# Kernel tuning notes

Hardware: AMD Instinct MI355X
Metric: run time of the kernel (lower is better)

## Reference

```python
import jax, jax.numpy as jnp
import numpy as np

B, T, D, K = 32, 2048, 1024, 31


def setup_inputs() -> dict:
    key = jax.random.key(0)
    ks = jax.random.split(key, 8)
    query = jax.random.normal(ks[0], (B, D), dtype=jnp.float32)
    memory = jax.random.normal(ks[1], (B, T, D), dtype=jnp.float32)
    prev_attn = jax.nn.softmax(jax.random.normal(ks[2], (B, T)), axis=-1).astype(jnp.float32)
    cum_attn = jax.random.uniform(ks[3], (B, T), dtype=jnp.float32)
    mask = jax.random.bernoulli(ks[4], 0.2, (B, T))
    mask = mask.at[:, 0].set(False)  # keep at least one valid position per row
    scale = 0.02
    Wq = jax.random.normal(ks[5], (D, D), dtype=jnp.float32) * scale    # torch Linear weight [out,in]
    Wm = jax.random.normal(ks[6], (D, D), dtype=jnp.float32) * scale
    k2 = jax.random.split(ks[7], 2)
    Wloc = jax.random.normal(k2[0], (D, 2, K), dtype=jnp.float32) * scale  # Conv1d weight [out_ch,in_ch,k]
    v = jax.random.normal(k2[1], (D,), dtype=jnp.float32) * scale          # Linear(d_model,1) weight squeezed
    return {"query": query, "memory": memory, "prev_attn": prev_attn,
            "cum_attn": cum_attn, "mask": mask,
            "Wq": Wq, "Wm": Wm, "Wloc": Wloc, "v": v}


def reference(query, memory, prev_attn, cum_attn, mask, Wq, Wm, Wloc, v):
    pad = Wloc.shape[-1] // 2
    # location features: [B,2,T] conv -> [B,D,T] -> [B,T,D]
    loc_in = jnp.stack([prev_attn, cum_attn], axis=1)
    loc = jax.lax.conv_general_dilated(
        loc_in, Wloc, window_strides=(1,), padding=[(pad, pad)],
        dimension_numbers=("NCW", "OIW", "NCW"))
    loc = jnp.transpose(loc, (0, 2, 1))                 # [B,T,D]
    q = (query @ Wq.T)[:, None, :]                      # [B,1,D]
    m = jnp.einsum("btd,ed->bte", memory, Wm)           # [B,T,D]
    e = jnp.einsum("btd,d->bt", jnp.tanh(q + m + loc), v)  # [B,T]
    e = jnp.where(mask, -jnp.inf, e)
    a = jax.nn.softmax(e, axis=1)                       # [B,T]
    ctx = jnp.einsum("bt,btd->bd", a, memory)           # [B,D]
    return ctx, a
```

## Files before the change

### kernel.cpp

```cpp
#include <hip/hip_runtime.h>
#include <math.h>

#define BATCH 32
#define T 2048
#define D 1024
#define KW 31
#define CPAD 15
#define KEXT 62
#define KTOT 1088
#define BM 128
#define BN 128
#define BK 32
#define NSTEP (KTOT / BK)

typedef __bf16 bf16_8 __attribute__((ext_vector_type(8)));
typedef __bf16 bf16_4 __attribute__((ext_vector_type(4)));
typedef float  f32x4  __attribute__((ext_vector_type(4)));

__device__ __forceinline__ float tanh_fast(float x) {
    return 1.f - 2.f * __builtin_amdgcn_rcpf(__expf(2.f * x) + 1.f);
}

__device__ __forceinline__ void glds16(const void* gsrc, void* ldst) {
    __builtin_amdgcn_global_load_lds(
        (const __attribute__((address_space(1))) unsigned int*)gsrc,
        (__attribute__((address_space(3))) unsigned int*)ldst, 16, 0, 0);
}

__global__ __launch_bounds__(256) void k_prep_b(const float* __restrict__ Wm,
                                                const float* __restrict__ Wloc,
                                                __bf16* __restrict__ Bext) {
    const int idx = blockIdx.x * 256 + threadIdx.x;
    const int d = idx / (KTOT / 4);
    const int kk = (idx % (KTOT / 4)) * 4;
    bf16_4 o;
    #pragma unroll
    for (int u = 0; u < 4; ++u) {
        const int k = kk + u;
        float val = 0.f;
        if (k < D) val = Wm[(size_t)d * D + k];
        else {
            const int j = k - D;
            if (j < KEXT) {
                const int c = (j >= KW) ? 1 : 0;
                const int kp = j - c * KW;
                val = Wloc[((size_t)d * 2 + c) * KW + kp];
            }
        }
        o[u] = (__bf16)val;
    }
    *(bf16_4*)(Bext + (size_t)d * KTOT + kk) = o;
}

__global__ __launch_bounds__(256) void k_prep_amem(const float* __restrict__ memory,
                                                   __bf16* __restrict__ Amem) {
    const int nvec = BATCH * T * (D / 8);
    for (int idx = blockIdx.x * 256 + threadIdx.x; idx < nvec; idx += gridDim.x * 256) {
        const int row = idx >> 7;
        const int c = (idx & 127) * 8;
        const float* src = memory + (size_t)row * D + c;
        const f32x4 lo = *(const f32x4*)src;
        const f32x4 hi = *(const f32x4*)(src + 4);
        bf16_8 o;
        #pragma unroll
        for (int u = 0; u < 4; ++u) { o[u] = (__bf16)lo[u]; o[u + 4] = (__bf16)hi[u]; }
        *(bf16_8*)(Amem + (size_t)row * KTOT + c) = o;
    }
}

__global__ __launch_bounds__(256) void k_prep_aloc(const float* __restrict__ prev,
                                                   const float* __restrict__ cum,
                                                   __bf16* __restrict__ Amem) {
    const int idx = blockIdx.x * 256 + threadIdx.x;
    const int row = idx >> 4;
    const int j0 = (idx & 15) * 4;
    const int b = row >> 11;
    const int t = row & (T - 1);
    bf16_4 o;
    #pragma unroll
    for (int u = 0; u < 4; ++u) {
        const int j = j0 + u;
        float val = 0.f;
        if (j < KEXT) {
            const int c = (j >= KW) ? 1 : 0;
            const int kp = j - c * KW;
            const int ts = t + kp - CPAD;
            if (ts >= 0 && ts < T)
                val = (c ? cum : prev)[(size_t)b * T + ts];
        }
        o[u] = (__bf16)val;
    }
    *(bf16_4*)(Amem + (size_t)row * KTOT + D + j0) = o;
}

__global__ __launch_bounds__(256) void k_q(const float* __restrict__ query,
                                           const float* __restrict__ Wq,
                                           float* __restrict__ qout) {
    int b = blockIdx.y;
    int w = threadIdx.x >> 6;
    int lane = threadIdx.x & 63;
    int d = blockIdx.x * 4 + w;
    const float* qrow = query + (size_t)b * D;
    const float* wrow = Wq + (size_t)d * D;
    float s = 0.f;
    #pragma unroll
    for (int i = 0; i < D / 64; ++i) s += qrow[lane + i * 64] * wrow[lane + i * 64];
    #pragma unroll
    for (int off = 32; off > 0; off >>= 1) s += __shfl_down(s, off, 64);
    if (lane == 0) qout[(size_t)b * D + d] = s;
}

__global__ __launch_bounds__(256, 4) void k_gemm_e(
    const __bf16* __restrict__ Amem, const __bf16* __restrict__ Bext,
    const float* __restrict__ qv, const float* __restrict__ vvec,
    float* __restrict__ e_part) {
    __shared__ bf16_8 As[2][512];
    __shared__ bf16_8 Bs[2][512];

    const int t0 = blockIdx.x * BM;
    const int d0 = blockIdx.y * BN;
    const int b  = blockIdx.z;
    const int tid  = threadIdx.x;
    const int lane = tid & 63;
    const int w    = tid >> 6;
    const int wr   = w >> 1, wc = w & 1;
    const int q    = lane >> 4, m = lane & 15;

    f32x4 acc[4][4] = {};

    const int g0 = w, g1 = w + 4;
    const __bf16* aptr0 = Amem + ((size_t)b * T + t0 + g0 * 16 + m) * KTOT + q * 8;
    const __bf16* aptr1 = Amem + ((size_t)b * T + t0 + g1 * 16 + m) * KTOT + q * 8;
    const __bf16* bptr0 = Bext + (size_t)(d0 + g0 * 16 + m) * KTOT + q * 8;
    const __bf16* bptr1 = Bext + (size_t)(d0 + g1 * 16 + m) * KTOT + q * 8;

    glds16(aptr0, &As[0][g0 * 64]);
    glds16(aptr1, &As[0][g1 * 64]);
    glds16(bptr0, &Bs[0][g0 * 64]);
    glds16(bptr1, &Bs[0][g1 * 64]);
    __syncthreads();

    for (int k = 0; k < NSTEP; ++k) {
        const int p = k & 1;
        const int kn = k + 1;
        if (kn < NSTEP) {
            const int kk = kn * BK;
            glds16(aptr0 + kk, &As[p ^ 1][g0 * 64]);
            glds16(aptr1 + kk, &As[p ^ 1][g1 * 64]);
            glds16(bptr0 + kk, &Bs[p ^ 1][g0 * 64]);
            glds16(bptr1 + kk, &Bs[p ^ 1][g1 * 64]);
        }
        bf16_8 bfr[4];
        #pragma unroll
        for (int j = 0; j < 4; ++j) bfr[j] = Bs[p][(wc * 4 + j) * 64 + lane];
        #pragma unroll
        for (int i = 0; i < 4; ++i) {
            const bf16_8 af = As[p][(wr * 4 + i) * 64 + lane];
            #pragma unroll
            for (int j = 0; j < 4; ++j)
                acc[i][j] = __builtin_amdgcn_mfma_f32_16x16x32_bf16(af, bfr[j], acc[i][j], 0, 0, 0);
        }
        __syncthreads();
    }

    float qreg[4], vreg[4];
    #pragma unroll
    for (int j = 0; j < 4; ++j) {
        const int d = d0 + wc * 64 + j * 16 + m;
        qreg[j] = qv[(size_t)b * D + d];
        vreg[j] = vvec[d];
    }
    const int dch = blockIdx.y * 2 + wc;
    #pragma unroll
    for (int i = 0; i < 4; ++i) {
        #pragma unroll
        for (int r = 0; r < 4; ++r) {
            float s = 0.f;
            #pragma unroll
            for (int j = 0; j < 4; ++j)
                s += tanh_fast(acc[i][j][r] + qreg[j]) * vreg[j];
            #pragma unroll
            for (int off = 8; off > 0; off >>= 1)
                s += __shfl_down(s, off, 16);
            if (m == 0) {
                const int t = t0 + wr * 64 + i * 16 + q * 4 + r;
                e_part[((size_t)b * T + t) * 16 + dch] = s;
            }
        }
    }
}

__global__ __launch_bounds__(256) void k_softmax(const float* __restrict__ e_part,
                                                 const int* __restrict__ mask,
                                                 float* __restrict__ aout) {
    const int b = blockIdx.x;
    const int tid = threadIdx.x;
    __shared__ float red[256];
    float ev[8];
    float lmax = -INFINITY;
    #pragma unroll
    for (int i = 0; i < 8; ++i) {
        const int t = tid + i * 256;
        const float* p = e_part + ((size_t)b * T + t) * 16;
        float s = 0.f;
        #pragma unroll
        for (int c = 0; c < 16; ++c) s += p[c];
        if (mask[(size_t)b * T + t] != 0) s = -INFINITY;
        ev[i] = s;
        lmax = fmaxf(lmax, s);
    }
    red[tid] = lmax; __syncthreads();
    for (int off = 128; off > 0; off >>= 1) {
        if (tid < off) red[tid] = fmaxf(red[tid], red[tid + off]);
        __syncthreads();
    }
    const float mx = red[0]; __syncthreads();
    float lsum = 0.f;
    #pragma unroll
    for (int i = 0; i < 8; ++i) {
        const float x = expf(ev[i] - mx);
        ev[i] = x;
        lsum += x;
    }
    red[tid] = lsum; __syncthreads();
    for (int off = 128; off > 0; off >>= 1) {
        if (tid < off) red[tid] += red[tid + off];
        __syncthreads();
    }
    const float inv = 1.f / red[0];
    #pragma unroll
    for (int i = 0; i < 8; ++i)
        aout[(size_t)b * T + tid + i * 256] = ev[i] * inv;
}

__global__ __launch_bounds__(256) void k_ctx_part(const float* __restrict__ memory,
                                                  const float* __restrict__ a,
                                                  float* __restrict__ ctx_part) {
    const int b = blockIdx.x;
    const int tc = blockIdx.y;
    const int d4 = threadIdx.x * 4;
    f32x4 acc = {0.f, 0.f, 0.f, 0.f};
    const float* mb = memory + ((size_t)b * T + (size_t)tc * 64) * D;
    const float* ab = a + (size_t)b * T + (size_t)tc * 64;
    #pragma unroll 4
    for (int t = 0; t < 64; ++t) {
        const float wgt = ab[t];
        const f32x4 m4 = *(const f32x4*)(mb + (size_t)t * D + d4);
        acc += wgt * m4;
    }
    *(f32x4*)(ctx_part + ((size_t)(b * 32 + tc)) * D + d4) = acc;
}

__global__ __launch_bounds__(256) void k_ctx_red(const float* __restrict__ ctx_part,
                                                 float* __restrict__ ctx) {
    const int idx = blockIdx.x * 256 + threadIdx.x;
    const int b = idx >> 10, d = idx & 1023;
    float s = 0.f;
    #pragma unroll
    for (int tc = 0; tc < 32; ++tc) s += ctx_part[((size_t)(b * 32 + tc)) * D + d];
    ctx[idx] = s;
}

extern "C" void kernel_launch(void* const* d_in, const int* in_sizes, int n_in,
                              void* d_out, int out_size, void* d_ws, size_t ws_size,
                              hipStream_t stream) {
    const float* query  = (const float*)d_in[0];
    const float* memory = (const float*)d_in[1];
    const float* prev   = (const float*)d_in[2];
    const float* cum    = (const float*)d_in[3];
    const int*   mask   = (const int*)d_in[4];
    const float* Wq     = (const float*)d_in[5];
    const float* Wm     = (const float*)d_in[6];
    const float* Wloc   = (const float*)d_in[7];
    const float* v      = (const float*)d_in[8];

    float* out = (float*)d_out;
    float* ctx = out;
    float* a   = out + BATCH * D;

    char* ws = (char*)d_ws;
    float*  qv       = (float*)(ws + 0);
    float*  e_part   = (float*)(ws + 131072);
    float*  ctx_part = (float*)(ws + 4325376);
    __bf16* Bext     = (__bf16*)(ws + 8519680);
    __bf16* Amem     = (__bf16*)(ws + 10747904);

    k_prep_b<<<KTOT * D / (256 * 4), 256, 0, stream>>>(Wm, Wloc, Bext);
    k_prep_amem<<<8192, 256, 0, stream>>>(memory, Amem);
    k_prep_aloc<<<BATCH * T * 16 / 256, 256, 0, stream>>>(prev, cum, Amem);
    k_q<<<dim3(D / 4, BATCH), 256, 0, stream>>>(query, Wq, qv);
    k_gemm_e<<<dim3(T / BM, D / BN, BATCH), 256, 0, stream>>>(Amem, Bext, qv, v, e_part);
    k_softmax<<<BATCH, 256, 0, stream>>>(e_part, mask, a);
    k_ctx_part<<<dim3(BATCH, 32), 256, 0, stream>>>(memory, a, ctx_part);
    k_ctx_red<<<(BATCH * D) / 256, 256, 0, stream>>>(ctx_part, ctx);
}
```

Before: 732.4 us.

## Deepen GEMM A-tile prefetch with triple buffering and partial vmcnt waits

The bf16 GEMM mainloop now triple-buffers A tiles in LDS and prefetches them two steps ahead, while B stays double-buffered and is issued one step ahead. A targeted s_waitcnt vmcnt(2) plus a raw s_barrier replaces the full wait-and-sync per step, so one A prefetch can stay in flight across the barrier. The aim is to hide more global-load latency behind the MFMA work. The memory-to-bf16 prep kernel also converts 16 floats per thread with half as many blocks. The cost is extra LDS per block (one more A buffer), which could affect occupancy at the declared launch bounds, and the correctness of the hand-counted vmcnt ordering.

```diff
diff --git a/kernel.cpp b/kernel.cpp
--- a/kernel.cpp
+++ b/kernel.cpp
@@ -54,17 +54,24 @@
 
 __global__ __launch_bounds__(256) void k_prep_amem(const float* __restrict__ memory,
                                                    __bf16* __restrict__ Amem) {
-    const int nvec = BATCH * T * (D / 8);
+    const int nvec = BATCH * T * (D / 16);
     for (int idx = blockIdx.x * 256 + threadIdx.x; idx < nvec; idx += gridDim.x * 256) {
-        const int row = idx >> 7;
-        const int c = (idx & 127) * 8;
+        const int row = idx >> 6;
+        const int c = (idx & 63) * 16;
         const float* src = memory + (size_t)row * D + c;
-        const f32x4 lo = *(const f32x4*)src;
-        const f32x4 hi = *(const f32x4*)(src + 4);
-        bf16_8 o;
-        #pragma unroll
-        for (int u = 0; u < 4; ++u) { o[u] = (__bf16)lo[u]; o[u + 4] = (__bf16)hi[u]; }
-        *(bf16_8*)(Amem + (size_t)row * KTOT + c) = o;
+        const f32x4 a0 = *(const f32x4*)(src);
+        const f32x4 a1 = *(const f32x4*)(src + 4);
+        const f32x4 a2 = *(const f32x4*)(src + 8);
+        const f32x4 a3 = *(const f32x4*)(src + 12);
+        bf16_8 o0, o1;
+        #pragma unroll
+        for (int u = 0; u < 4; ++u) {
+            o0[u] = (__bf16)a0[u]; o0[u + 4] = (__bf16)a1[u];
+            o1[u] = (__bf16)a2[u]; o1[u + 4] = (__bf16)a3[u];
+        }
+        __bf16* dst = Amem + (size_t)row * KTOT + c;
+        *(bf16_8*)(dst) = o0;
+        *(bf16_8*)(dst + 8) = o1;
     }
 }
 
@@ -114,7 +121,7 @@
     const __bf16* __restrict__ Amem, const __bf16* __restrict__ Bext,
     const float* __restrict__ qv, const float* __restrict__ vvec,
     float* __restrict__ e_part) {
-    __shared__ bf16_8 As[2][512];
+    __shared__ bf16_8 As[3][512];
     __shared__ bf16_8 Bs[2][512];
 
     const int t0 = blockIdx.x * BM;
@@ -134,34 +141,43 @@
     const __bf16* bptr0 = Bext + (size_t)(d0 + g0 * 16 + m) * KTOT + q * 8;
     const __bf16* bptr1 = Bext + (size_t)(d0 + g1 * 16 + m) * KTOT + q * 8;
 
-    glds16(aptr0, &As[0][g0 * 64]);
-    glds16(aptr1, &As[0][g1 * 64]);
-    glds16(bptr0, &Bs[0][g0 * 64]);
-    glds16(bptr1, &Bs[0][g1 * 64]);
-    __syncthreads();
-
-    for (int k = 0; k < NSTEP; ++k) {
-        const int p = k & 1;
-        const int kn = k + 1;
-        if (kn < NSTEP) {
-            const int kk = kn * BK;
-            glds16(aptr0 + kk, &As[p ^ 1][g0 * 64]);
-            glds16(aptr1 + kk, &As[p ^ 1][g1 * 64]);
-            glds16(bptr0 + kk, &Bs[p ^ 1][g0 * 64]);
-            glds16(bptr1 + kk, &Bs[p ^ 1][g1 * 64]);
-        }
+    auto compute = [&](int pA, int pB) {
         bf16_8 bfr[4];
         #pragma unroll
-        for (int j = 0; j < 4; ++j) bfr[j] = Bs[p][(wc * 4 + j) * 64 + lane];
+        for (int j = 0; j < 4; ++j) bfr[j] = Bs[pB][(wc * 4 + j) * 64 + lane];
         #pragma unroll
         for (int i = 0; i < 4; ++i) {
-            const bf16_8 af = As[p][(wr * 4 + i) * 64 + lane];
+            const bf16_8 af = As[pA][(wr * 4 + i) * 64 + lane];
             #pragma unroll
             for (int j = 0; j < 4; ++j)
                 acc[i][j] = __builtin_amdgcn_mfma_f32_16x16x32_bf16(af, bfr[j], acc[i][j], 0, 0, 0);
         }
-        __syncthreads();
-    }
+    };
+
+    glds16(aptr0,      &As[0][g0 * 64]);
+    glds16(aptr1,      &As[0][g1 * 64]);
+    glds16(bptr0,      &Bs[0][g0 * 64]);
+    glds16(bptr1,      &Bs[0][g1 * 64]);
+    glds16(aptr0 + BK, &As[1][g0 * 64]);
+    glds16(aptr1 + BK, &As[1][g1 * 64]);
+
+    #pragma unroll 1
+    for (int k = 0; k < NSTEP - 1; ++k) {
+        asm volatile("s_waitcnt vmcnt(2)" ::: "memory");
+        __builtin_amdgcn_s_barrier();
+        const int kb1 = k + 1;
+        glds16(bptr0 + kb1 * BK, &Bs[kb1 & 1][g0 * 64]);
+        glds16(bptr1 + kb1 * BK, &Bs[kb1 & 1][g1 * 64]);
+        const int ka2 = k + 2;
+        if (ka2 < NSTEP) {
+            glds16(aptr0 + ka2 * BK, &As[ka2 % 3][g0 * 64]);
+            glds16(aptr1 + ka2 * BK, &As[ka2 % 3][g1 * 64]);
+        }
+        compute(k % 3, k & 1);
+    }
+    asm volatile("s_waitcnt vmcnt(0)" ::: "memory");
+    __builtin_amdgcn_s_barrier();
+    compute((NSTEP - 1) % 3, (NSTEP - 1) & 1);
 
     float qreg[4], vreg[4];
     #pragma unroll
@@ -286,7 +302,7 @@
     __bf16* Amem     = (__bf16*)(ws + 10747904);
 
     k_prep_b<<<KTOT * D / (256 * 4), 256, 0, stream>>>(Wm, Wloc, Bext);
-    k_prep_amem<<<8192, 256, 0, stream>>>(memory, Amem);
+    k_prep_amem<<<4096, 256, 0, stream>>>(memory, Amem);
     k_prep_aloc<<<BATCH * T * 16 / 256, 256, 0, stream>>>(prev, cum, Amem);
     k_q<<<dim3(D / 4, BATCH), 256, 0, stream>>>(query, Wq, qv);
     k_gemm_e<<<dim3(T / BM, D / BN, BATCH), 256, 0, stream>>>(Amem, Bext, qv, v, e_part);
```

Result: no change. 729.0 us (-0.5%).
